# Optimization experiments

Hardware: AMD Instinct MI355X
Metric: run time of the kernel (lower is better)

The kernel has to match this reference:

```python
import jax, jax.numpy as jnp
import numpy as np

B, N, DIM, H, DH, MLP, DEPTH = 32, 256, 384, 6, 64, 1536, 12
INNER = H * DH
LN_EPS = 1e-5
LS_INIT = 0.1  # LayerScale init_eps for depth <= 18


def setup_inputs() -> dict:
    key = jax.random.key(0)
    ks = jax.random.split(key, 10)
    f = lambda k, shape, s=0.02: jax.random.normal(k, shape, jnp.float32) * s
    return {
        "x": jax.random.normal(ks[0], (B, N, DIM), jnp.float32),
        "ln1_g": jnp.ones((DEPTH, DIM), jnp.float32),
        "ln1_b": jnp.zeros((DEPTH, DIM), jnp.float32),
        "wq": f(ks[1], (DEPTH, DIM, INNER)),
        "wkv": f(ks[2], (DEPTH, DIM, 2 * INNER)),
        "scale": jnp.full((DEPTH, H), DH ** -0.5, jnp.float32),  # learned per-head scale
        "mix_pre": f(ks[3], (DEPTH, H, H), 1.0),   # torch.randn init
        "mix_post": f(ks[4], (DEPTH, H, H), 1.0),
        "wo": f(ks[5], (DEPTH, INNER, DIM)),
        "bo": jnp.zeros((DEPTH, DIM), jnp.float32),
        "ls1": jnp.full((DEPTH, DIM), LS_INIT, jnp.float32),
        "ln2_g": jnp.ones((DEPTH, DIM), jnp.float32),
        "ln2_b": jnp.zeros((DEPTH, DIM), jnp.float32),
        "w1": f(ks[6], (DEPTH, DIM, MLP)),
        "b1": jnp.zeros((DEPTH, MLP), jnp.float32),
        "w2": f(ks[7], (DEPTH, MLP, DIM)),
        "b2": jnp.zeros((DEPTH, DIM), jnp.float32),
        "ls2": jnp.full((DEPTH, DIM), LS_INIT, jnp.float32),
    }


def _layernorm(x, g, b):
    mu = jnp.mean(x, axis=-1, keepdims=True)
    var = jnp.mean(jnp.square(x - mu), axis=-1, keepdims=True)
    return (x - mu) * jax.lax.rsqrt(var + LN_EPS) * g + b


def reference(x, ln1_g, ln1_b, wq, wkv, scale, mix_pre, mix_post, wo, bo, ls1,
              ln2_g, ln2_b, w1, b1, w2, b2, ls2):
    diag = jnp.eye(N, dtype=bool)  # self-attention diagonal mask

    def block(x, p):
        (g1, bb1, wq_, wkv_, sc, mp, mq, wo_, bo_, l1,
         g2, bb2, w1_, b1_, w2_, b2_, l2) = p
        # --- talking-heads attention (PreNorm + LayerScale + residual) ---
        y = _layernorm(x, g1, bb1)
        q = (y @ wq_).reshape(B, N, H, DH).transpose(0, 2, 1, 3)       # b h n d
        kv = y @ wkv_
        k, v = jnp.split(kv, 2, axis=-1)
        k = k.reshape(B, N, H, DH).transpose(0, 2, 1, 3)
        v = v.reshape(B, N, H, DH).transpose(0, 2, 1, 3)
        dots = jnp.einsum('bhid,bhjd->bhij', q, k) * sc[None, :, None, None]
        dots = jnp.einsum('bhij,hg->bgij', dots, mp)                   # pre-softmax head mix
        dots = jnp.where(diag, -jnp.inf, dots)                         # mask self positions
        attn = jax.nn.softmax(dots, axis=-1)
        attn = jnp.einsum('bhij,hg->bgij', attn, mq)                   # post-softmax head mix
        o = jnp.einsum('bhij,bhjd->bhid', attn, v)
        o = o.transpose(0, 2, 1, 3).reshape(B, N, INNER) @ wo_ + bo_
        x = o * l1 + x
        # --- FFN (PreNorm + LayerScale + residual) ---
        y2 = _layernorm(x, g2, bb2)
        h = jax.nn.gelu(y2 @ w1_ + b1_, approximate=False)
        x = (h @ w2_ + b2_) * l2 + x
        return x, None

    params = (ln1_g, ln1_b, wq, wkv, scale, mix_pre, mix_post, wo, bo, ls1,
              ln2_g, ln2_b, w1, b1, w2, b2, ls2)
    x, _ = jax.lax.scan(block, x, params)
    return x
```

## Files before the change

### kernel.cpp

```cpp
#include <hip/hip_runtime.h>
#include <hip/hip_bf16.h>
#include <math.h>

#define B_ 32
#define N_ 256
#define DIM_ 384
#define H_ 6
#define DH_ 64
#define INNER_ 384
#define MLP_ 1536
#define DEPTH_ 12
#define T_ (B_ * N_)

typedef __bf16 bf16x8 __attribute__((ext_vector_type(8)));
typedef __bf16 bf16x4 __attribute__((ext_vector_type(4)));
typedef float f32x4 __attribute__((ext_vector_type(4)));

typedef const __attribute__((address_space(1))) void* gas_ptr;
typedef __attribute__((address_space(3))) void* las_ptr;

#define WQKV_OFF 0
#define WO_OFF   (1152 * 384)
#define W1_OFF   (WO_OFF + 384 * 384)
#define W2_OFF   (W1_OFF + 1536 * 384)
#define WBUF_ELEMS (W2_OFF + 384 * 1536)

__global__ __launch_bounds__(256) void convert_w_all(
    const float* __restrict__ wq0, const float* __restrict__ wkv0,
    const float* __restrict__ wo0, const float* __restrict__ w10,
    const float* __restrict__ w20, __bf16* __restrict__ wbuf0)
{
    __shared__ float til[64][65];
    int t = blockIdx.x;
    int l = t / 432; t -= l * 432;
    const float* wq  = wq0  + (size_t)l * DIM_ * INNER_;
    const float* wkv = wkv0 + (size_t)l * DIM_ * 2 * INNER_;
    const float* wo  = wo0  + (size_t)l * INNER_ * DIM_;
    const float* w1  = w10  + (size_t)l * DIM_ * MLP_;
    const float* w2  = w20  + (size_t)l * MLP_ * DIM_;
    __bf16* wbuf = wbuf0 + (size_t)l * WBUF_ELEMS;

    int lane = threadIdx.x & 63, seg = threadIdx.x >> 6;
    const float* src; __bf16* dst;
    int Ns, sc, dK, dR, k0;
    if (t < 108) {
        int nt = t / 6, kt = t % 6;
        int n0 = nt * 64; k0 = kt * 64;
        dst = wbuf + WQKV_OFF; dK = 384; dR = n0;
        if (n0 < 384) { src = wq;  Ns = 384; sc = n0; }
        else          { src = wkv; Ns = 768; sc = n0 - 384; }
    } else if (t < 144) {
        int u = t - 108; int nt = u / 6, kt = u % 6;
        src = wo; Ns = 384; sc = nt * 64;
        dst = wbuf + WO_OFF; dK = 384; dR = nt * 64; k0 = kt * 64;
    } else if (t < 288) {
        int u = t - 144; int nt = u / 6, kt = u % 6;
        src = w1; Ns = 1536; sc = nt * 64;
        dst = wbuf + W1_OFF; dK = 384; dR = nt * 64; k0 = kt * 64;
    } else {
        int u = t - 288; int nt = u / 24, kt = u % 24;
        src = w2; Ns = 384; sc = nt * 64;
        dst = wbuf + W2_OFF; dK = 1536; dR = nt * 64; k0 = kt * 64;
    }
    #pragma unroll
    for (int r = 0; r < 16; ++r) {
        int i = seg * 16 + r;
        til[i][lane] = src[(size_t)(k0 + i) * Ns + sc + lane];
    }
    __syncthreads();
    #pragma unroll
    for (int r = 0; r < 16; ++r) {
        int i = seg * 16 + r;
        dst[(size_t)(dR + i) * dK + k0 + lane] = (__bf16)til[lane][i];
    }
}

__global__ __launch_bounds__(64) void ln1w(
    const float* __restrict__ x, const float* __restrict__ g,
    const float* __restrict__ b, __bf16* __restrict__ y)
{
    size_t row = blockIdx.x;
    int lane = threadIdx.x;
    const float* xr = x + row * DIM_;
    float v[6];
    #pragma unroll
    for (int s = 0; s < 6; ++s) v[s] = xr[lane + 64 * s];
    float sum = 0.f;
    #pragma unroll
    for (int s = 0; s < 6; ++s) sum += v[s];
    #pragma unroll
    for (int o = 32; o > 0; o >>= 1) sum += __shfl_xor(sum, o);
    float mu = sum * (1.0f / DIM_);
    float var = 0.f;
    #pragma unroll
    for (int s = 0; s < 6; ++s) { float d = v[s] - mu; var += d * d; }
    #pragma unroll
    for (int o = 32; o > 0; o >>= 1) var += __shfl_xor(var, o);
    float rs = rsqrtf(var * (1.0f / DIM_) + 1e-5f);
    __bf16* yr = y + row * DIM_;
    #pragma unroll
    for (int s = 0; s < 6; ++s) {
        int e = lane + 64 * s;
        yr[e] = (__bf16)((v[s] - mu) * rs * g[e] + b[e]);
    }
}

template<int MODE, int K, int BM, int BN, int BK, int NT>
__global__ __launch_bounds__(256) void gemmt(
    const __bf16* __restrict__ A, const __bf16* __restrict__ Bt,
    const float* __restrict__ bias, const float* __restrict__ ls,
    float* __restrict__ xf, __bf16* __restrict__ out,
    __bf16* __restrict__ oq, __bf16* __restrict__ ok, __bf16* __restrict__ ov,
    int Nn)
{
    constexpr int WM = BM / 32, WN = BN / 32;
    constexpr int KS = BK / 32;
    constexpr int MT = T_ / BM;
    constexpr int nIter = K / BK;
    constexpr bool SWZ = (BK == 64);
    constexpr int RPI = 512 / BK;
    constexpr int CL  = BK / 8;
    constexpr int LPT = BM / (4 * RPI) + BN / (4 * RPI);
    static_assert(LPT == 4, "vmcnt formula assumes 4 loads per tile per wave");

    __shared__ __align__(16) __bf16 sA[2][BM * BK];
    __shared__ __align__(16) __bf16 sB[2][BN * BK];

    int id = blockIdx.x;
    constexpr int nxg = (MT * NT) / 8;
    int wg = (id & 7) * nxg + (id >> 3);
    int bm = (wg / NT) * BM;
    int bn = (wg % NT) * BN;
    int tid = threadIdx.x;
    int lane = tid & 63, wid = tid >> 6;
    int wm = (wid & 1) * (BM / 2), wn = (wid >> 1) * (BN / 2);
    int fm = lane & 15, fq = lane >> 4;

    f32x4 acc[WM][WN] = {};

    int lr = lane / CL, lc = lane % CL;
    int lcs = SWZ ? (lc ^ lr) : lc;
    const __bf16* aBase = A + (size_t)(bm + wid * RPI + lr) * K + lcs * 8;
    const __bf16* bBase = Bt + (size_t)(bn + wid * RPI + lr) * K + lcs * 8;

    auto stage = [&](int buf, int kk) {
        #pragma unroll
        for (int qI = 0; qI < BM / (4 * RPI); ++qI)
            __builtin_amdgcn_global_load_lds(
                (gas_ptr)(aBase + (size_t)(qI * 4 * RPI) * K + kk),
                (las_ptr)&sA[buf][qI * 2048 + wid * 512], 16, 0, 0);
        #pragma unroll
        for (int qI = 0; qI < BN / (4 * RPI); ++qI)
            __builtin_amdgcn_global_load_lds(
                (gas_ptr)(bBase + (size_t)(qI * 4 * RPI) * K + kk),
                (las_ptr)&sB[buf][qI * 2048 + wid * 512], 16, 0, 0);
    };

    stage(0, 0);

    #pragma unroll
    for (int i = 0; i < nIter; ++i) {
        int cur = i & 1;
        if (i + 1 < nIter) {
            stage(cur ^ 1, (i + 1) * BK);
            asm volatile("s_waitcnt vmcnt(4)" ::: "memory");
        } else {
            asm volatile("s_waitcnt vmcnt(0)" ::: "memory");
        }
        __builtin_amdgcn_s_barrier();
        __builtin_amdgcn_sched_barrier(0);

        bf16x8 af[KS][WM], bfr[KS][WN];
        #pragma unroll
        for (int ks = 0; ks < KS; ++ks) {
            #pragma unroll
            for (int ii = 0; ii < WM; ++ii) {
                int row = wm + ii * 16 + fm;
                int c = SWZ ? (((ks * 4 + fq) ^ (row & 7)) * 8) : (ks * 32 + fq * 8);
                af[ks][ii] = *(const bf16x8*)&sA[cur][row * BK + c];
            }
            #pragma unroll
            for (int jj = 0; jj < WN; ++jj) {
                int row = wn + jj * 16 + fm;
                int c = SWZ ? (((ks * 4 + fq) ^ (row & 7)) * 8) : (ks * 32 + fq * 8);
                bfr[ks][jj] = *(const bf16x8*)&sB[cur][row * BK + c];
            }
        }
        #pragma unroll
        for (int ks = 0; ks < KS; ++ks)
            #pragma unroll
            for (int ii = 0; ii < WM; ++ii)
                #pragma unroll
                for (int jj = 0; jj < WN; ++jj)
                    acc[ii][jj] = __builtin_amdgcn_mfma_f32_16x16x32_bf16(
                        af[ks][ii], bfr[ks][jj], acc[ii][jj], 0, 0, 0);

        if (i + 1 < nIter) {
            asm volatile("s_waitcnt lgkmcnt(0)" ::: "memory");
            __builtin_amdgcn_sched_barrier(0);
            __builtin_amdgcn_s_barrier();
            __builtin_amdgcn_sched_barrier(0);
        }
    }

    #pragma unroll
    for (int jj = 0; jj < WN; ++jj) {
        int col = bn + wn + jj * 16 + fm;
        float bv = (MODE != 0) ? bias[col] : 0.0f;
        float lv = (MODE == 2) ? ls[col] : 0.0f;
        #pragma unroll
        for (int ii = 0; ii < WM; ++ii) {
            #pragma unroll
            for (int r = 0; r < 4; ++r) {
                int row = bm + wm + ii * 16 + fq * 4 + r;
                float v = acc[ii][jj][r];
                if (MODE == 0) {
                    if (col < 384)      oq[(size_t)row * 384 + col] = (__bf16)v;
                    else if (col < 768) ok[(size_t)row * 384 + col - 384] = (__bf16)v;
                    else {
                        int bb = row >> 8, tj = row & 255;
                        ov[((size_t)bb * 384 + (col - 768)) * 256 + tj] = (__bf16)v;
                    }
                } else if (MODE == 1) {
                    v += bv;
                    v = 0.5f * v * (1.0f + erff(v * 0.70710678118f));
                    out[(size_t)row * Nn + col] = (__bf16)v;
                } else {
                    size_t idx = (size_t)row * Nn + col;
                    xf[idx] = (v + bv) * lv + xf[idx];
                }
            }
        }
    }
}

#define PAD_S 264

__global__ __launch_bounds__(384) void attn_mfma(
    const __bf16* __restrict__ q, const __bf16* __restrict__ kb,
    const __bf16* __restrict__ vT, const float* __restrict__ scale,
    const float* __restrict__ mp, const float* __restrict__ mq,
    __bf16* __restrict__ o)
{
    __shared__ __bf16 sbuf[96][PAD_S];

    int id = blockIdx.x;
    int b = (id & 7) + ((id >> 3) & 3) * 8;
    int i0 = (id >> 5) * 16;
    int tid = threadIdx.x;
    int lane = tid & 63, wid = tid >> 6;
    int fm = lane & 15, fq = lane >> 4;

    int h = wid;
    bf16x8 qf[2];
    #pragma unroll
    for (int ks = 0; ks < 2; ++ks)
        qf[ks] = *(const bf16x8*)&q[(size_t)(b * 256 + i0 + fm) * 384 + h * 64 + ks * 32 + fq * 8];
    #pragma unroll 4
    for (int jt = 0; jt < 16; ++jt) {
        f32x4 a = {};
        #pragma unroll
        for (int ks = 0; ks < 2; ++ks) {
            bf16x8 bfr = *(const bf16x8*)&kb[(size_t)(b * 256 + jt * 16 + fm) * 384 + h * 64 + ks * 32 + fq * 8];
            a = __builtin_amdgcn_mfma_f32_16x16x32_bf16(qf[ks], bfr, a, 0, 0, 0);
        }
        #pragma unroll
        for (int r = 0; r < 4; ++r)
            sbuf[h * 16 + fq * 4 + r][jt * 16 + fm] = (__bf16)a[r];
    }

    float mps[36], mqs[36];
    #pragma unroll
    for (int t = 0; t < 36; ++t) { mps[t] = mp[t] * scale[t / 6]; mqs[t] = mq[t]; }

    __syncthreads();

    for (int i = wid; i < 16; i += 6) {
        float sv[6][4];
        #pragma unroll
        for (int h2 = 0; h2 < 6; ++h2) {
            bf16x4 v4 = *(const bf16x4*)&sbuf[h2 * 16 + i][lane * 4];
            #pragma unroll
            for (int c = 0; c < 4; ++c) sv[h2][c] = (float)v4[c];
        }
        int drow = i0 + i;
        float pv[6][4];
        #pragma unroll
        for (int g2 = 0; g2 < 6; ++g2) {
            float t0[4];
            #pragma unroll
            for (int c = 0; c < 4; ++c) {
                float r2 = 0.f;
                #pragma unroll
                for (int h2 = 0; h2 < 6; ++h2) r2 += sv[h2][c] * mps[h2 * 6 + g2];
                t0[c] = (lane * 4 + c == drow) ? -1e30f : r2;
            }
            float m = fmaxf(fmaxf(t0[0], t0[1]), fmaxf(t0[2], t0[3]));
            #pragma unroll
            for (int off = 32; off > 0; off >>= 1) m = fmaxf(m, __shfl_xor(m, off));
            float e0 = __expf(t0[0] - m), e1 = __expf(t0[1] - m);
            float e2 = __expf(t0[2] - m), e3 = __expf(t0[3] - m);
            float s = e0 + e1 + e2 + e3;
            #pragma unroll
            for (int off = 32; off > 0; off >>= 1) s += __shfl_xor(s, off);
            float inv = 1.0f / s;
            pv[g2][0] = e0 * inv; pv[g2][1] = e1 * inv;
            pv[g2][2] = e2 * inv; pv[g2][3] = e3 * inv;
        }
        #pragma unroll
        for (int g2 = 0; g2 < 6; ++g2) {
            bf16x4 w4;
            #pragma unroll
            for (int c = 0; c < 4; ++c) {
                float r2 = 0.f;
                #pragma unroll
                for (int h2 = 0; h2 < 6; ++h2) r2 += pv[h2][c] * mqs[h2 * 6 + g2];
                w4[c] = (__bf16)r2;
            }
            *(bf16x4*)&sbuf[g2 * 16 + i][lane * 4] = w4;
        }
    }
    __syncthreads();

    int gg = wid;
    f32x4 acco[4] = {};
    #pragma unroll
    for (int jc = 0; jc < 4; ++jc) {
        #pragma unroll
        for (int ks = 0; ks < 2; ++ks) {
            bf16x8 af = *(const bf16x8*)&sbuf[gg * 16 + fm][jc * 64 + ks * 32 + fq * 8];
            #pragma unroll
            for (int nt = 0; nt < 4; ++nt) {
                bf16x8 bfr = *(const bf16x8*)&vT[(size_t)(b * 384 + gg * 64 + nt * 16 + fm) * 256 + jc * 64 + ks * 32 + fq * 8];
                acco[nt] = __builtin_amdgcn_mfma_f32_16x16x32_bf16(af, bfr, acco[nt], 0, 0, 0);
            }
        }
    }
    #pragma unroll
    for (int nt = 0; nt < 4; ++nt)
        #pragma unroll
        for (int r = 0; r < 4; ++r)
            o[(size_t)(b * 256 + i0 + fq * 4 + r) * 384 + gg * 64 + nt * 16 + fm] = (__bf16)acco[nt][r];
}

extern "C" void kernel_launch(void* const* d_in, const int* in_sizes, int n_in,
                              void* d_out, int out_size, void* d_ws, size_t ws_size,
                              hipStream_t stream) {
    const float* x      = (const float*)d_in[0];
    const float* ln1_g  = (const float*)d_in[1];
    const float* ln1_b  = (const float*)d_in[2];
    const float* wq     = (const float*)d_in[3];
    const float* wkv    = (const float*)d_in[4];
    const float* scale  = (const float*)d_in[5];
    const float* mixp   = (const float*)d_in[6];
    const float* mixq   = (const float*)d_in[7];
    const float* wo     = (const float*)d_in[8];
    const float* bo     = (const float*)d_in[9];
    const float* ls1    = (const float*)d_in[10];
    const float* ln2_g  = (const float*)d_in[11];
    const float* ln2_b  = (const float*)d_in[12];
    const float* w1     = (const float*)d_in[13];
    const float* b1     = (const float*)d_in[14];
    const float* w2     = (const float*)d_in[15];
    const float* b2     = (const float*)d_in[16];
    const float* ls2    = (const float*)d_in[17];

    char* ws = (char*)d_ws;
    float*  xf = (float*)ws;                      ws += (size_t)T_ * DIM_ * 4;
    __bf16* y  = (__bf16*)ws;                     ws += (size_t)T_ * DIM_ * 2;
    __bf16* q  = (__bf16*)ws;                     ws += (size_t)T_ * DIM_ * 2;
    __bf16* kb = (__bf16*)ws;                     ws += (size_t)T_ * DIM_ * 2;
    __bf16* vT = (__bf16*)ws;                     ws += (size_t)T_ * DIM_ * 2;
    __bf16* o  = (__bf16*)ws;                     ws += (size_t)T_ * DIM_ * 2;
    __bf16* wbuf = (__bf16*)ws;                   ws += (size_t)WBUF_ELEMS * DEPTH_ * 2;
    __bf16* h  = q;

    size_t nBytes = (size_t)T_ * DIM_ * sizeof(float);
    hipMemcpyAsync(xf, x, nBytes, hipMemcpyDeviceToDevice, stream);

    convert_w_all<<<432 * DEPTH_, 256, 0, stream>>>(wq, wkv, wo, w1, w2, wbuf);

    for (int l = 0; l < DEPTH_; ++l) {
        __bf16* wl = wbuf + (size_t)l * WBUF_ELEMS;

        ln1w<<<T_, 64, 0, stream>>>(xf, ln1_g + (size_t)l * DIM_, ln1_b + (size_t)l * DIM_, y);

        gemmt<0, 384, 128, 128, 32, 9><<<576, 256, 0, stream>>>(
            y, wl + WQKV_OFF, nullptr, nullptr, nullptr, nullptr,
            q, kb, vT, 1152);

        attn_mfma<<<512, 384, 0, stream>>>(
            q, kb, vT, scale + (size_t)l * H_,
            mixp + (size_t)l * H_ * H_, mixq + (size_t)l * H_ * H_, o);

        gemmt<2, 384, 64, 64, 64, 6><<<768, 256, 0, stream>>>(
            o, wl + WO_OFF, bo + (size_t)l * DIM_, ls1 + (size_t)l * DIM_,
            xf, nullptr, nullptr, nullptr, nullptr, DIM_);

        ln1w<<<T_, 64, 0, stream>>>(xf, ln2_g + (size_t)l * DIM_, ln2_b + (size_t)l * DIM_, y);

        gemmt<1, 384, 128, 128, 32, 12><<<768, 256, 0, stream>>>(
            y, wl + W1_OFF, b1 + (size_t)l * MLP_, nullptr,
            nullptr, h, nullptr, nullptr, nullptr, MLP_);

        gemmt<2, 1536, 64, 64, 64, 6><<<768, 256, 0, stream>>>(
            h, wl + W2_OFF, b2 + (size_t)l * DIM_, ls2 + (size_t)l * DIM_,
            xf, nullptr, nullptr, nullptr, nullptr, DIM_);
    }

    hipMemcpyAsync(d_out, xf, nBytes, hipMemcpyDeviceToDevice, stream);
}
```

Baseline: 1.629 ms.

## Fuse output projection and residual into attention kernel; pack 4 LN rows per block

The attention kernel now stages its 16x384 output tile in swizzled LDS and multiplies it by the Wo weights with MFMA inside the same block. It then applies bias, LayerScale and the residual update to xf directly, which removes the separate Wo GEMM launch and the round trip of the o buffer through global memory. The workspace is reorganised so q/k/vT alias the h buffer. Separately, the LayerNorm kernel processes four rows per 256-thread block instead of one row per 64-thread block, which reduces the block count. The fused GEMM reads Wo from global memory without LDS tiling, and each block's six waves compute only a 16-row tile, so Wo reuse is lower than in the tiled GEMM.

```diff
diff --git a/kernel.cpp b/kernel.cpp
--- a/kernel.cpp
+++ b/kernel.cpp
@@ -75,12 +75,12 @@
     }
 }
 
-__global__ __launch_bounds__(64) void ln1w(
+__global__ __launch_bounds__(256) void ln1w(
     const float* __restrict__ x, const float* __restrict__ g,
     const float* __restrict__ b, __bf16* __restrict__ y)
 {
-    size_t row = blockIdx.x;
-    int lane = threadIdx.x;
+    size_t row = blockIdx.x * 4 + (threadIdx.x >> 6);
+    int lane = threadIdx.x & 63;
     const float* xr = x + row * DIM_;
     float v[6];
     #pragma unroll
@@ -121,7 +121,7 @@
     constexpr int RPI = 512 / BK;
     constexpr int CL  = BK / 8;
     constexpr int LPT = BM / (4 * RPI) + BN / (4 * RPI);
-    static_assert(LPT == 4, "vmcnt formula assumes 4 loads per tile per wave");
+    static_assert(LPT == 4, "vmcnt literals assume 4 loads per tile per wave");
 
     __shared__ __align__(16) __bf16 sA[2][BM * BK];
     __shared__ __align__(16) __bf16 sB[2][BN * BK];
@@ -240,9 +240,10 @@
     const __bf16* __restrict__ q, const __bf16* __restrict__ kb,
     const __bf16* __restrict__ vT, const float* __restrict__ scale,
     const float* __restrict__ mp, const float* __restrict__ mq,
-    __bf16* __restrict__ o)
+    const __bf16* __restrict__ wot, const float* __restrict__ bo,
+    const float* __restrict__ ls, float* __restrict__ xf)
 {
-    __shared__ __bf16 sbuf[96][PAD_S];
+    __shared__ __align__(16) __bf16 sbuf[96][PAD_S];
 
     int id = blockIdx.x;
     int b = (id & 7) + ((id >> 3) & 3) * 8;
@@ -336,11 +337,39 @@
             }
         }
     }
+
+    __syncthreads();
+    __bf16* oB = &sbuf[0][0];
     #pragma unroll
     for (int nt = 0; nt < 4; ++nt)
         #pragma unroll
-        for (int r = 0; r < 4; ++r)
-            o[(size_t)(b * 256 + i0 + fq * 4 + r) * 384 + gg * 64 + nt * 16 + fm] = (__bf16)acco[nt][r];
+        for (int r = 0; r < 4; ++r) {
+            int row = fq * 4 + r;
+            int col = gg * 64 + nt * 16 + fm;
+            oB[row * 384 + (((col >> 3) ^ (row & 7)) << 3) + (col & 7)] = (__bf16)acco[nt][r];
+        }
+    __syncthreads();
+
+    f32x4 acc2[4] = {};
+    #pragma unroll
+    for (int ks = 0; ks < 12; ++ks) {
+        bf16x8 af = *(const bf16x8*)&oB[fm * 384 + (((ks * 4 + fq) ^ (fm & 7)) << 3)];
+        #pragma unroll
+        for (int nt = 0; nt < 4; ++nt) {
+            bf16x8 bfr = *(const bf16x8*)&wot[(size_t)(gg * 64 + nt * 16 + fm) * 384 + ks * 32 + fq * 8];
+            acc2[nt] = __builtin_amdgcn_mfma_f32_16x16x32_bf16(af, bfr, acc2[nt], 0, 0, 0);
+        }
+    }
+    #pragma unroll
+    for (int nt = 0; nt < 4; ++nt) {
+        int col = gg * 64 + nt * 16 + fm;
+        float bv = bo[col], lv = ls[col];
+        #pragma unroll
+        for (int r = 0; r < 4; ++r) {
+            size_t idx = (size_t)(b * 256 + i0 + fq * 4 + r) * 384 + col;
+            xf[idx] = (acc2[nt][r] + bv) * lv + xf[idx];
+        }
+    }
 }
 
 extern "C" void kernel_launch(void* const* d_in, const int* in_sizes, int n_in,
@@ -368,12 +397,12 @@
     char* ws = (char*)d_ws;
     float*  xf = (float*)ws;                      ws += (size_t)T_ * DIM_ * 4;
     __bf16* y  = (__bf16*)ws;                     ws += (size_t)T_ * DIM_ * 2;
-    __bf16* q  = (__bf16*)ws;                     ws += (size_t)T_ * DIM_ * 2;
-    __bf16* kb = (__bf16*)ws;                     ws += (size_t)T_ * DIM_ * 2;
-    __bf16* vT = (__bf16*)ws;                     ws += (size_t)T_ * DIM_ * 2;
-    __bf16* o  = (__bf16*)ws;                     ws += (size_t)T_ * DIM_ * 2;
+    __bf16* q  = (__bf16*)ws;
+    __bf16* kb = q  + (size_t)T_ * DIM_;
+    __bf16* vT = kb + (size_t)T_ * DIM_;
+    __bf16* h  = q;
+    ws += (size_t)T_ * MLP_ * 2;
     __bf16* wbuf = (__bf16*)ws;                   ws += (size_t)WBUF_ELEMS * DEPTH_ * 2;
-    __bf16* h  = q;
 
     size_t nBytes = (size_t)T_ * DIM_ * sizeof(float);
     hipMemcpyAsync(xf, x, nBytes, hipMemcpyDeviceToDevice, stream);
@@ -383,7 +412,7 @@
     for (int l = 0; l < DEPTH_; ++l) {
         __bf16* wl = wbuf + (size_t)l * WBUF_ELEMS;
 
-        ln1w<<<T_, 64, 0, stream>>>(xf, ln1_g + (size_t)l * DIM_, ln1_b + (size_t)l * DIM_, y);
+        ln1w<<<T_ / 4, 256, 0, stream>>>(xf, ln1_g + (size_t)l * DIM_, ln1_b + (size_t)l * DIM_, y);
 
         gemmt<0, 384, 128, 128, 32, 9><<<576, 256, 0, stream>>>(
             y, wl + WQKV_OFF, nullptr, nullptr, nullptr, nullptr,
@@ -391,13 +420,10 @@
 
         attn_mfma<<<512, 384, 0, stream>>>(
             q, kb, vT, scale + (size_t)l * H_,
-            mixp + (size_t)l * H_ * H_, mixq + (size_t)l * H_ * H_, o);
-
-        gemmt<2, 384, 64, 64, 64, 6><<<768, 256, 0, stream>>>(
-            o, wl + WO_OFF, bo + (size_t)l * DIM_, ls1 + (size_t)l * DIM_,
-            xf, nullptr, nullptr, nullptr, nullptr, DIM_);
-
-        ln1w<<<T_, 64, 0, stream>>>(xf, ln2_g + (size_t)l * DIM_, ln2_b + (size_t)l * DIM_, y);
+            mixp + (size_t)l * H_ * H_, mixq + (size_t)l * H_ * H_,
+            wl + WO_OFF, bo + (size_t)l * DIM_, ls1 + (size_t)l * DIM_, xf);
+
+        ln1w<<<T_ / 4, 256, 0, stream>>>(xf, ln2_g + (size_t)l * DIM_, ln2_b + (size_t)l * DIM_, y);
 
         gemmt<1, 384, 128, 128, 32, 12><<<768, 256, 0, stream>>>(
             y, wl + W1_OFF, b1 + (size_t)l * MLP_, nullptr,
```

After: 1.720 ms. 1.06x slower.
